# Kernel tuning notes

Hardware: AMD Instinct MI355X
Metric: run time of the kernel (lower is better)

Reference implementation:

```python
import jax, jax.numpy as jnp
import numpy as np

N_NODES = 100000
N_EDGES = 3200000
NUM_FEATURES = 256
HIDDEN = 16
NUM_CLASSES = 40


def gcn_conv(x, edge_index, W, b, num_nodes):
    """PyG GCNConv: linear -> add self-loops -> symmetric deg norm -> scatter-add -> bias."""
    x = x @ W  # [N, out]
    loop = jnp.arange(num_nodes)
    src = jnp.concatenate([edge_index[0], loop])  # messages flow src -> dst
    dst = jnp.concatenate([edge_index[1], loop])
    # degree of target nodes (with self-loops)
    deg = jax.ops.segment_sum(jnp.ones_like(dst, dtype=x.dtype), dst,
                              num_segments=num_nodes)
    dinv = jnp.where(deg > 0, jax.lax.rsqrt(deg), 0.0)
    norm = dinv[src] * dinv[dst]  # [E+N]
    out = jax.ops.segment_sum(x[src] * norm[:, None], dst,
                              num_segments=num_nodes)
    return out + b


def setup_inputs() -> dict:
    key = jax.random.key(0)
    k1, k2, k3, k4 = jax.random.split(key, 4)
    x = jax.random.normal(k1, (N_NODES, NUM_FEATURES), dtype=jnp.float32)
    edge_index = jax.random.randint(k2, (2, N_EDGES), 0, N_NODES, dtype=jnp.int64)
    W1 = jax.random.normal(k3, (NUM_FEATURES, HIDDEN), dtype=jnp.float32) / np.sqrt(NUM_FEATURES)
    b1 = jnp.zeros((HIDDEN,), dtype=jnp.float32)
    W2 = jax.random.normal(k4, (HIDDEN, NUM_CLASSES), dtype=jnp.float32) / np.sqrt(HIDDEN)
    b2 = jnp.zeros((NUM_CLASSES,), dtype=jnp.float32)
    return {"x": x, "edge_index": edge_index, "W1": W1, "b1": b1, "W2": W2, "b2": b2}


def reference(x, edge_index, W1, b1, W2, b2):
    h = jax.nn.relu(gcn_conv(x, edge_index, W1, b1, N_NODES))
    return gcn_conv(h, edge_index, W2, b2, N_NODES)
```

## Files before the change

kernel.cpp:

```cpp
#include <hip/hip_runtime.h>
#include <hip/hip_fp16.h>

#define N_NODES   100000
#define N_EDGES   3200000
#define F_IN      256
#define HID       16
#define NCLS      40

#define CHUNK     16384
#define NBLK      ((N_EDGES + CHUNK - 1) / CHUNK)
#define B2SHIFT   9
#define NB2       ((N_NODES + 511) >> B2SHIFT)

__global__ __launch_bounds__(256) void hist_kernel(const int* __restrict__ ei,
                                                   int* __restrict__ hist_blk) {
    __shared__ int h[NB2];
    int blk = blockIdx.x, t = threadIdx.x;
    for (int i = t; i < NB2; i += 256) h[i] = 0;
    __syncthreads();
    int e0 = blk * CHUNK;
    int eN = min(CHUNK, N_EDGES - e0);
    for (int i = t; i < eN; i += 256)
        atomicAdd(&h[ei[N_EDGES + e0 + i] >> B2SHIFT], 1);
    __syncthreads();
    for (int i = t; i < NB2; i += 256) hist_blk[i * NBLK + blk] = h[i];
}

__global__ __launch_bounds__(256) void rowscan_kernel(int* __restrict__ hist_blk,
                                                      int* __restrict__ rowsum) {
    __shared__ int part[256];
    int b = blockIdx.x, t = threadIdx.x;
    int v = (t < NBLK) ? hist_blk[b * NBLK + t] : 0;
    part[t] = v;
    __syncthreads();
    for (int off = 1; off < 256; off <<= 1) {
        int u = (t >= off) ? part[t - off] : 0;
        __syncthreads();
        part[t] += u;
        __syncthreads();
    }
    if (t < NBLK) hist_blk[b * NBLK + t] = part[t] - v;
    if (t == 255) rowsum[b] = part[255];
}

__global__ __launch_bounds__(256) void basescan_kernel(const int* __restrict__ rowsum,
                                                       int* __restrict__ bucket_base) {
    __shared__ int part[256];
    int t = threadIdx.x;
    int v = (t < NB2) ? rowsum[t] : 0;
    part[t] = v;
    __syncthreads();
    for (int off = 1; off < 256; off <<= 1) {
        int u = (t >= off) ? part[t - off] : 0;
        __syncthreads();
        part[t] += u;
        __syncthreads();
    }
    if (t < NB2) bucket_base[t] = part[t] - v;
}

__global__ __launch_bounds__(256) void bin2_kernel(const int* __restrict__ ei,
                                                   const int* __restrict__ hist_blk,
                                                   const int* __restrict__ bucket_base,
                                                   int* __restrict__ buf) {
    __shared__ int cur[NB2];
    int blk = blockIdx.x, t = threadIdx.x;
    for (int i = t; i < NB2; i += 256)
        cur[i] = bucket_base[i] + hist_blk[i * NBLK + blk];
    __syncthreads();
    int e0 = blk * CHUNK;
    int eN = min(CHUNK, N_EDGES - e0);
    for (int i = t; i < eN; i += 256) {
        int d = ei[N_EDGES + e0 + i];
        int s = ei[e0 + i];
        int pos = atomicAdd(&cur[d >> B2SHIFT], 1);
        buf[pos] = ((d & 511) << 17) | s;
    }
}

__global__ __launch_bounds__(512) void build_kernel(const int* __restrict__ buf,
                                                    const int* __restrict__ bucket_base,
                                                    const int* __restrict__ rowsum,
                                                    int* __restrict__ rowptr,
                                                    float* __restrict__ dinv,
                                                    int* __restrict__ csr_src) {
    __shared__ int hist[512], offs[512], cur[512];
    int b = blockIdx.x, t = threadIdx.x;
    int base = bucket_base[b];
    int cnt  = rowsum[b];
    hist[t] = 0;
    __syncthreads();
    for (int i = t; i < cnt; i += 512)
        atomicAdd(&hist[buf[base + i] >> 17], 1);
    __syncthreads();
    int v = hist[t];
    offs[t] = v;
    __syncthreads();
    for (int off = 1; off < 512; off <<= 1) {
        int u = (t >= off) ? offs[t - off] : 0;
        __syncthreads();
        offs[t] += u;
        __syncthreads();
    }
    int ex = offs[t] - v;
    int n = (b << B2SHIFT) + t;
    if (n < N_NODES) {
        rowptr[n] = base + ex;
        dinv[n]   = rsqrtf((float)(v + 1));
    }
    if (b == 0 && t == 0) rowptr[N_NODES] = N_EDGES;
    cur[t] = ex;
    __syncthreads();
    for (int i = t; i < cnt; i += 512) {
        int p = buf[base + i];
        int pos = atomicAdd(&cur[p >> 17], 1);
        csr_src[base + pos] = p & 0x1FFFF;
    }
}

__global__ __launch_bounds__(256) void gemm1_kernel(const float* __restrict__ x,
                                                    const float* __restrict__ W1,
                                                    const float* __restrict__ dinv,
                                                    __half* __restrict__ y1h) {
    __shared__ float W1s[F_IN * HID];
    int t = threadIdx.x;
    #pragma unroll
    for (int i = 0; i < (F_IN * HID) / 256; i++) W1s[t + i * 256] = W1[t + i * 256];
    __syncthreads();

    int n = blockIdx.x * 256 + t;
    if (n >= N_NODES) return;

    const float4* xr = (const float4*)(x + (size_t)n * F_IN);
    float acc[HID];
    #pragma unroll
    for (int h = 0; h < HID; h++) acc[h] = 0.f;

    #pragma unroll 4
    for (int k4 = 0; k4 < F_IN / 4; k4++) {
        float4 xv = xr[k4];
        int k = k4 * 4;
        #pragma unroll
        for (int h = 0; h < HID; h++) {
            acc[h] += xv.x * W1s[(k + 0) * HID + h] + xv.y * W1s[(k + 1) * HID + h]
                    + xv.z * W1s[(k + 2) * HID + h] + xv.w * W1s[(k + 3) * HID + h];
        }
    }
    float dv = dinv[n];
    __half2 hp[8];
    #pragma unroll
    for (int j = 0; j < 8; j++)
        hp[j] = __float22half2_rn(make_float2(acc[2 * j] * dv, acc[2 * j + 1] * dv));
    float4* o = (float4*)(y1h + (size_t)n * HID);
    o[0] = ((float4*)hp)[0];
    o[1] = ((float4*)hp)[1];
}

__global__ void gather1_kernel(const int* __restrict__ rowptr, const int* __restrict__ csr_src,
                               const __half* __restrict__ y1h, const float* __restrict__ b1,
                               const float* __restrict__ dinv, __half* __restrict__ zh) {
    int idx = blockIdx.x * blockDim.x + threadIdx.x;
    if (idx >= N_NODES * 2) return;
    int n = idx >> 1, q = idx & 1;
    int beg = rowptr[n], end = rowptr[n + 1];
    const float4* tab = (const float4*)y1h;
    float acc[8];
    {
        float4 v = tab[(size_t)n * 2 + q];
        const __half2* a = (const __half2*)&v;
        #pragma unroll
        for (int j = 0; j < 4; j++) {
            float2 f = __half22float2(a[j]);
            acc[2 * j] = f.x; acc[2 * j + 1] = f.y;
        }
    }
    int e = beg;
    for (; e + 1 < end; e += 2) {
        int s0 = csr_src[e], s1 = csr_src[e + 1];
        float4 v0 = tab[(size_t)s0 * 2 + q];
        float4 v1 = tab[(size_t)s1 * 2 + q];
        const __half2* a0 = (const __half2*)&v0;
        const __half2* a1 = (const __half2*)&v1;
        #pragma unroll
        for (int j = 0; j < 4; j++) {
            float2 f0 = __half22float2(a0[j]);
            float2 f1 = __half22float2(a1[j]);
            acc[2 * j]     += f0.x + f1.x;
            acc[2 * j + 1] += f0.y + f1.y;
        }
    }
    if (e < end) {
        int s = csr_src[e];
        float4 v = tab[(size_t)s * 2 + q];
        const __half2* a = (const __half2*)&v;
        #pragma unroll
        for (int j = 0; j < 4; j++) {
            float2 f = __half22float2(a[j]);
            acc[2 * j] += f.x; acc[2 * j + 1] += f.y;
        }
    }
    float dv = dinv[n];
    __half2 outp[4];
    #pragma unroll
    for (int j = 0; j < 4; j++) {
        float2 r;
        r.x = fmaxf(dv * acc[2 * j]     + b1[q * 8 + 2 * j],     0.f) * dv;
        r.y = fmaxf(dv * acc[2 * j + 1] + b1[q * 8 + 2 * j + 1], 0.f) * dv;
        outp[j] = __float22half2_rn(r);
    }
    *(float4*)(zh + (size_t)n * HID + q * 8) = *(float4*)outp;
}

__global__ void gather2_kernel(const int* __restrict__ rowptr, const int* __restrict__ csr_src,
                               const __half* __restrict__ zh, float* __restrict__ agg2) {
    int idx = blockIdx.x * blockDim.x + threadIdx.x;
    if (idx >= N_NODES * 2) return;
    int n = idx >> 1, q = idx & 1;
    int beg = rowptr[n], end = rowptr[n + 1];
    const float4* tab = (const float4*)zh;
    float acc[8];
    {
        float4 v = tab[(size_t)n * 2 + q];
        const __half2* a = (const __half2*)&v;
        #pragma unroll
        for (int j = 0; j < 4; j++) {
            float2 f = __half22float2(a[j]);
            acc[2 * j] = f.x; acc[2 * j + 1] = f.y;
        }
    }
    int e = beg;
    for (; e + 1 < end; e += 2) {
        int s0 = csr_src[e], s1 = csr_src[e + 1];
        float4 v0 = tab[(size_t)s0 * 2 + q];
        float4 v1 = tab[(size_t)s1 * 2 + q];
        const __half2* a0 = (const __half2*)&v0;
        const __half2* a1 = (const __half2*)&v1;
        #pragma unroll
        for (int j = 0; j < 4; j++) {
            float2 f0 = __half22float2(a0[j]);
            float2 f1 = __half22float2(a1[j]);
            acc[2 * j]     += f0.x + f1.x;
            acc[2 * j + 1] += f0.y + f1.y;
        }
    }
    if (e < end) {
        int s = csr_src[e];
        float4 v = tab[(size_t)s * 2 + q];
        const __half2* a = (const __half2*)&v;
        #pragma unroll
        for (int j = 0; j < 4; j++) {
            float2 f = __half22float2(a[j]);
            acc[2 * j] += f.x; acc[2 * j + 1] += f.y;
        }
    }
    float4* o = (float4*)(agg2 + (size_t)n * HID + q * 8);
    o[0] = make_float4(acc[0], acc[1], acc[2], acc[3]);
    o[1] = make_float4(acc[4], acc[5], acc[6], acc[7]);
}

__global__ __launch_bounds__(320) void gemm2_kernel(const float* __restrict__ agg2,
                                                    const float* __restrict__ W2,
                                                    const float* __restrict__ dinv,
                                                    const float* __restrict__ b2,
                                                    float* __restrict__ out) {
    __shared__ float W2s[HID * NCLS];
    __shared__ float hs[8 * HID];
    __shared__ float b2s[NCLS];
    int t = threadIdx.x;
    for (int i = t; i < HID * NCLS; i += 320) W2s[i] = W2[i];
    if (t < NCLS) b2s[t] = b2[t];
    int n0 = blockIdx.x * 8;
    if (t < 8 * HID) {
        int n = n0 + t / HID;
        hs[t] = (n < N_NODES) ? agg2[(size_t)n * HID + (t % HID)] : 0.f;
    }
    __syncthreads();
    int ln = t / NCLS, c = t % NCLS;
    int n = n0 + ln;
    if (ln >= 8 || n >= N_NODES) return;
    float s = 0.f;
    #pragma unroll
    for (int h = 0; h < HID; h++) s += hs[ln * HID + h] * W2s[h * NCLS + c];
    out[(size_t)n * NCLS + c] = dinv[n] * s + b2s[c];
}

extern "C" void kernel_launch(void* const* d_in, const int* in_sizes, int n_in,
                              void* d_out, int out_size, void* d_ws, size_t ws_size,
                              hipStream_t stream) {
    const float* x   = (const float*)d_in[0];
    const int*   ei  = (const int*)  d_in[1];
    const float* W1  = (const float*)d_in[2];
    const float* b1  = (const float*)d_in[3];
    const float* W2  = (const float*)d_in[4];
    const float* b2  = (const float*)d_in[5];
    float* out = (float*)d_out;

    char* ws = (char*)d_ws;
    size_t off = 0;
    int*   hist_blk    = (int*)(ws + off); off += (size_t)NB2 * NBLK * 4;
    int*   rowsum      = (int*)(ws + off); off += (size_t)NB2 * 4;
    int*   bucket_base = (int*)(ws + off); off += (size_t)NB2 * 4;
    off = (off + 15) & ~(size_t)15;
    int*    rowptr  = (int*)   (ws + off); off += (size_t)(N_NODES + 1) * 4;
    off = (off + 15) & ~(size_t)15;
    float*  dinv    = (float*) (ws + off); off += (size_t)N_NODES * 4;
    int*    csr_src = (int*)   (ws + off); off += (size_t)N_EDGES * 4;
    int*    buf     = (int*)   (ws + off); off += (size_t)N_EDGES * 4;
    __half* y1h     = (__half*)(ws + off); off += (size_t)N_NODES * HID * 2;
    __half* zh      = (__half*)(ws + off); off += (size_t)N_NODES * HID * 2;
    float*  agg2    = (float*) (ws + off); off += (size_t)N_NODES * HID * 4;

    hist_kernel    <<<NBLK, 256, 0, stream>>>(ei, hist_blk);
    rowscan_kernel <<<NB2, 256, 0, stream>>>(hist_blk, rowsum);
    basescan_kernel<<<1, 256, 0, stream>>>(rowsum, bucket_base);
    bin2_kernel    <<<NBLK, 256, 0, stream>>>(ei, hist_blk, bucket_base, buf);
    build_kernel   <<<NB2, 512, 0, stream>>>(buf, bucket_base, rowsum, rowptr, dinv, csr_src);

    gemm1_kernel  <<<(N_NODES + 255) / 256, 256, 0, stream>>>(x, W1, dinv, y1h);
    gather1_kernel<<<(N_NODES * 2 + 255) / 256, 256, 0, stream>>>(rowptr, csr_src, y1h, b1, dinv, zh);
    gather2_kernel<<<(N_NODES * 2 + 255) / 256, 256, 0, stream>>>(rowptr, csr_src, zh, agg2);
    gemm2_kernel  <<<(N_NODES + 7) / 8, 320, 0, stream>>>(agg2, W2, dinv, b2, out);
}
```

Before: 389.9 us.

## Use 16-lane groups per node in gathers, fuse GEMM2, cache bucket in LDS

The gather kernels now assign 16 lanes to each destination node instead of 2. Each lane walks a strided slice of the neighbor list, loads full 32-byte rows, and the partial sums are combined with xor-shuffle reductions. This spreads work across edges rather than feature halves, which should improve memory-level parallelism and load balance. The second gather is fused with the W2 projection and bias, removing the agg2 round trip and one launch. build_kernel also caches its bucket of packed edges in LDS so the second pass avoids a global reread. The costs are a larger LDS footprint in build_kernel, more shuffle traffic, and idle lanes when a node has few edges.

```diff
diff --git a/kernel.cpp b/kernel.cpp
--- a/kernel.cpp
+++ b/kernel.cpp
@@ -11,6 +11,7 @@
 #define NBLK      ((N_EDGES + CHUNK - 1) / CHUNK)
 #define B2SHIFT   9
 #define NB2       ((N_NODES + 511) >> B2SHIFT)
+#define BCAP      17408
 
 __global__ __launch_bounds__(256) void hist_kernel(const int* __restrict__ ei,
                                                    int* __restrict__ hist_blk) {
@@ -84,14 +85,18 @@
                                                     int* __restrict__ rowptr,
                                                     float* __restrict__ dinv,
                                                     int* __restrict__ csr_src) {
+    __shared__ int lbuf[BCAP];
     __shared__ int hist[512], offs[512], cur[512];
     int b = blockIdx.x, t = threadIdx.x;
     int base = bucket_base[b];
     int cnt  = rowsum[b];
     hist[t] = 0;
     __syncthreads();
-    for (int i = t; i < cnt; i += 512)
-        atomicAdd(&hist[buf[base + i] >> 17], 1);
+    for (int i = t; i < cnt; i += 512) {
+        int v = buf[base + i];
+        if (i < BCAP) lbuf[i] = v;
+        atomicAdd(&hist[v >> 17], 1);
+    }
     __syncthreads();
     int v = hist[t];
     offs[t] = v;
@@ -112,7 +117,7 @@
     cur[t] = ex;
     __syncthreads();
     for (int i = t; i < cnt; i += 512) {
-        int p = buf[base + i];
+        int p = (i < BCAP) ? lbuf[i] : buf[base + i];
         int pos = atomicAdd(&cur[p >> 17], 1);
         csr_src[base + pos] = p & 0x1FFFF;
     }
@@ -156,132 +161,105 @@
     o[1] = ((float4*)hp)[1];
 }
 
-__global__ void gather1_kernel(const int* __restrict__ rowptr, const int* __restrict__ csr_src,
-                               const __half* __restrict__ y1h, const float* __restrict__ b1,
-                               const float* __restrict__ dinv, __half* __restrict__ zh) {
-    int idx = blockIdx.x * blockDim.x + threadIdx.x;
-    if (idx >= N_NODES * 2) return;
-    int n = idx >> 1, q = idx & 1;
+__device__ __forceinline__ void acc_row(const float4* __restrict__ tab, int s, float* acc) {
+    float4 v0 = tab[(size_t)s * 2 + 0];
+    float4 v1 = tab[(size_t)s * 2 + 1];
+    const __half2* a0 = (const __half2*)&v0;
+    const __half2* a1 = (const __half2*)&v1;
+    #pragma unroll
+    for (int j = 0; j < 4; j++) {
+        float2 f0 = __half22float2(a0[j]);
+        float2 f1 = __half22float2(a1[j]);
+        acc[2 * j]         += f0.x;
+        acc[2 * j + 1]     += f0.y;
+        acc[8 + 2 * j]     += f1.x;
+        acc[8 + 2 * j + 1] += f1.y;
+    }
+}
+
+__global__ __launch_bounds__(256) void gather1_kernel(const int* __restrict__ rowptr,
+                                                      const int* __restrict__ csr_src,
+                                                      const __half* __restrict__ y1h,
+                                                      const float* __restrict__ b1,
+                                                      const float* __restrict__ dinv,
+                                                      __half* __restrict__ zh) {
+    int n   = blockIdx.x * 16 + (threadIdx.x >> 4);
+    int sub = threadIdx.x & 15;
+    const float4* tab = (const float4*)y1h;
     int beg = rowptr[n], end = rowptr[n + 1];
-    const float4* tab = (const float4*)y1h;
-    float acc[8];
-    {
-        float4 v = tab[(size_t)n * 2 + q];
-        const __half2* a = (const __half2*)&v;
+    float acc[16];
+    #pragma unroll
+    for (int i = 0; i < 16; i++) acc[i] = 0.f;
+    if (sub == 0) acc_row(tab, n, acc);
+    for (int e = beg + sub; e < end; e += 16)
+        acc_row(tab, csr_src[e], acc);
+    #pragma unroll
+    for (int m = 1; m < 16; m <<= 1) {
+        #pragma unroll
+        for (int i = 0; i < 16; i++) acc[i] += __shfl_xor(acc[i], m, 16);
+    }
+    if (sub < 2) {
+        float dv = dinv[n];
+        const float4* b1q = (const float4*)b1;
+        float4 ba = b1q[sub * 2], bb = b1q[sub * 2 + 1];
+        const float* bp = (sub == 0) ? (const float*)&ba : (const float*)&ba;
+        float bv[8] = {ba.x, ba.y, ba.z, ba.w, bb.x, bb.y, bb.z, bb.w};
+        (void)bp;
+        __half2 outp[4];
         #pragma unroll
         for (int j = 0; j < 4; j++) {
-            float2 f = __half22float2(a[j]);
-            acc[2 * j] = f.x; acc[2 * j + 1] = f.y;
+            float2 r;
+            r.x = fmaxf(dv * acc[sub * 8 + 2 * j]     + bv[2 * j],     0.f) * dv;
+            r.y = fmaxf(dv * acc[sub * 8 + 2 * j + 1] + bv[2 * j + 1], 0.f) * dv;
+            outp[j] = __float22half2_rn(r);
         }
-    }
-    int e = beg;
-    for (; e + 1 < end; e += 2) {
-        int s0 = csr_src[e], s1 = csr_src[e + 1];
-        float4 v0 = tab[(size_t)s0 * 2 + q];
-        float4 v1 = tab[(size_t)s1 * 2 + q];
-        const __half2* a0 = (const __half2*)&v0;
-        const __half2* a1 = (const __half2*)&v1;
-        #pragma unroll
-        for (int j = 0; j < 4; j++) {
-            float2 f0 = __half22float2(a0[j]);
-            float2 f1 = __half22float2(a1[j]);
-            acc[2 * j]     += f0.x + f1.x;
-            acc[2 * j + 1] += f0.y + f1.y;
-        }
-    }
-    if (e < end) {
-        int s = csr_src[e];
-        float4 v = tab[(size_t)s * 2 + q];
-        const __half2* a = (const __half2*)&v;
-        #pragma unroll
-        for (int j = 0; j < 4; j++) {
-            float2 f = __half22float2(a[j]);
-            acc[2 * j] += f.x; acc[2 * j + 1] += f.y;
-        }
-    }
-    float dv = dinv[n];
-    __half2 outp[4];
-    #pragma unroll
-    for (int j = 0; j < 4; j++) {
-        float2 r;
-        r.x = fmaxf(dv * acc[2 * j]     + b1[q * 8 + 2 * j],     0.f) * dv;
-        r.y = fmaxf(dv * acc[2 * j + 1] + b1[q * 8 + 2 * j + 1], 0.f) * dv;
-        outp[j] = __float22half2_rn(r);
-    }
-    *(float4*)(zh + (size_t)n * HID + q * 8) = *(float4*)outp;
-}
-
-__global__ void gather2_kernel(const int* __restrict__ rowptr, const int* __restrict__ csr_src,
-                               const __half* __restrict__ zh, float* __restrict__ agg2) {
-    int idx = blockIdx.x * blockDim.x + threadIdx.x;
-    if (idx >= N_NODES * 2) return;
-    int n = idx >> 1, q = idx & 1;
-    int beg = rowptr[n], end = rowptr[n + 1];
-    const float4* tab = (const float4*)zh;
-    float acc[8];
-    {
-        float4 v = tab[(size_t)n * 2 + q];
-        const __half2* a = (const __half2*)&v;
-        #pragma unroll
-        for (int j = 0; j < 4; j++) {
-            float2 f = __half22float2(a[j]);
-            acc[2 * j] = f.x; acc[2 * j + 1] = f.y;
-        }
-    }
-    int e = beg;
-    for (; e + 1 < end; e += 2) {
-        int s0 = csr_src[e], s1 = csr_src[e + 1];
-        float4 v0 = tab[(size_t)s0 * 2 + q];
-        float4 v1 = tab[(size_t)s1 * 2 + q];
-        const __half2* a0 = (const __half2*)&v0;
-        const __half2* a1 = (const __half2*)&v1;
-        #pragma unroll
-        for (int j = 0; j < 4; j++) {
-            float2 f0 = __half22float2(a0[j]);
-            float2 f1 = __half22float2(a1[j]);
-            acc[2 * j]     += f0.x + f1.x;
-            acc[2 * j + 1] += f0.y + f1.y;
-        }
-    }
-    if (e < end) {
-        int s = csr_src[e];
-        float4 v = tab[(size_t)s * 2 + q];
-        const __half2* a = (const __half2*)&v;
-        #pragma unroll
-        for (int j = 0; j < 4; j++) {
-            float2 f = __half22float2(a[j]);
-            acc[2 * j] += f.x; acc[2 * j + 1] += f.y;
-        }
-    }
-    float4* o = (float4*)(agg2 + (size_t)n * HID + q * 8);
-    o[0] = make_float4(acc[0], acc[1], acc[2], acc[3]);
-    o[1] = make_float4(acc[4], acc[5], acc[6], acc[7]);
-}
-
-__global__ __launch_bounds__(320) void gemm2_kernel(const float* __restrict__ agg2,
-                                                    const float* __restrict__ W2,
-                                                    const float* __restrict__ dinv,
-                                                    const float* __restrict__ b2,
-                                                    float* __restrict__ out) {
+        *(float4*)(zh + (size_t)n * HID + sub * 8) = *(float4*)outp;
+    }
+}
+
+__global__ __launch_bounds__(256) void gather2_kernel(const int* __restrict__ rowptr,
+                                                      const int* __restrict__ csr_src,
+                                                      const __half* __restrict__ zh,
+                                                      const float* __restrict__ W2,
+                                                      const float* __restrict__ b2,
+                                                      const float* __restrict__ dinv,
+                                                      float* __restrict__ out) {
     __shared__ float W2s[HID * NCLS];
-    __shared__ float hs[8 * HID];
     __shared__ float b2s[NCLS];
     int t = threadIdx.x;
-    for (int i = t; i < HID * NCLS; i += 320) W2s[i] = W2[i];
+    for (int i = t; i < HID * NCLS; i += 256) W2s[i] = W2[i];
     if (t < NCLS) b2s[t] = b2[t];
-    int n0 = blockIdx.x * 8;
-    if (t < 8 * HID) {
-        int n = n0 + t / HID;
-        hs[t] = (n < N_NODES) ? agg2[(size_t)n * HID + (t % HID)] : 0.f;
-    }
-    __syncthreads();
-    int ln = t / NCLS, c = t % NCLS;
-    int n = n0 + ln;
-    if (ln >= 8 || n >= N_NODES) return;
-    float s = 0.f;
-    #pragma unroll
-    for (int h = 0; h < HID; h++) s += hs[ln * HID + h] * W2s[h * NCLS + c];
-    out[(size_t)n * NCLS + c] = dinv[n] * s + b2s[c];
+    __syncthreads();
+
+    int n   = blockIdx.x * 16 + (t >> 4);
+    int sub = t & 15;
+    const float4* tab = (const float4*)zh;
+    int beg = rowptr[n], end = rowptr[n + 1];
+    float acc[16];
+    #pragma unroll
+    for (int i = 0; i < 16; i++) acc[i] = 0.f;
+    if (sub == 0) acc_row(tab, n, acc);
+    for (int e = beg + sub; e < end; e += 16)
+        acc_row(tab, csr_src[e], acc);
+    #pragma unroll
+    for (int m = 1; m < 16; m <<= 1) {
+        #pragma unroll
+        for (int i = 0; i < 16; i++) acc[i] += __shfl_xor(acc[i], m, 16);
+    }
+    if (sub < 10) {
+        float dv = dinv[n];
+        int c0 = sub * 4;
+        float o0 = 0.f, o1 = 0.f, o2 = 0.f, o3 = 0.f;
+        #pragma unroll
+        for (int h = 0; h < HID; h++) {
+            float a = acc[h];
+            const float* w = &W2s[h * NCLS + c0];
+            o0 += a * w[0]; o1 += a * w[1]; o2 += a * w[2]; o3 += a * w[3];
+        }
+        float4 r = make_float4(dv * o0 + b2s[c0],     dv * o1 + b2s[c0 + 1],
+                               dv * o2 + b2s[c0 + 2], dv * o3 + b2s[c0 + 3]);
+        *(float4*)(out + (size_t)n * NCLS + c0) = r;
+    }
 }
 
 extern "C" void kernel_launch(void* const* d_in, const int* in_sizes, int n_in,
@@ -308,7 +286,6 @@
     int*    buf     = (int*)   (ws + off); off += (size_t)N_EDGES * 4;
     __half* y1h     = (__half*)(ws + off); off += (size_t)N_NODES * HID * 2;
     __half* zh      = (__half*)(ws + off); off += (size_t)N_NODES * HID * 2;
-    float*  agg2    = (float*) (ws + off); off += (size_t)N_NODES * HID * 4;
 
     hist_kernel    <<<NBLK, 256, 0, stream>>>(ei, hist_blk);
     rowscan_kernel <<<NB2, 256, 0, stream>>>(hist_blk, rowsum);
@@ -317,7 +294,6 @@
     build_kernel   <<<NB2, 512, 0, stream>>>(buf, bucket_base, rowsum, rowptr, dinv, csr_src);
 
     gemm1_kernel  <<<(N_NODES + 255) / 256, 256, 0, stream>>>(x, W1, dinv, y1h);
-    gather1_kernel<<<(N_NODES * 2 + 255) / 256, 256, 0, stream>>>(rowptr, csr_src, y1h, b1, dinv, zh);
-    gather2_kernel<<<(N_NODES * 2 + 255) / 256, 256, 0, stream>>>(rowptr, csr_src, zh, agg2);
-    gemm2_kernel  <<<(N_NODES + 7) / 8, 320, 0, stream>>>(agg2, W2, dinv, b2, out);
-}
+    gather1_kernel<<<N_NODES / 16, 256, 0, stream>>>(rowptr, csr_src, y1h, b1, dinv, zh);
+    gather2_kernel<<<N_NODES / 16, 256, 0, stream>>>(rowptr, csr_src, zh, W2, b2, dinv, out);
+}
```

After: 357.9 us. -8.2%, faster.
